# Kernel tuning notes

Measured on AMD Instinct MI355X. Metric: run time of the kernel, lower is better.

Reference implementation:

```python
import jax, jax.numpy as jnp
import numpy as np

B, DIM, D_IN, HID, N_HID_EXTRA = 65536, 128, 64, 512, 2  # num_hidden_layers=3 -> 2 extra hidden linears
LOG_SCALE_CLAMP = 2.0


def _mlp(x, Win, bin_, Whid, bhid, Wout, bout):
    # torch nn.Linear: y = x @ W.T + b
    h = jax.nn.relu(x @ Win.T + bin_)
    for i in range(Whid.shape[0]):  # fixed small layer loop
        h = jax.nn.relu(h @ Whid[i].T + bhid[i])
    return h @ Wout.T + bout


def setup_inputs() -> dict:
    key = jax.random.key(0)
    ks = jax.random.split(key, 13)
    w = lambda k, shp: (jax.random.normal(k, shp, dtype=jnp.float32) * 0.05)
    d_out = DIM - D_IN
    return {
        "z": jax.random.normal(ks[0], (B, DIM), dtype=jnp.float32),
        "s_Win": w(ks[1], (HID, D_IN)),   "s_bin": jnp.zeros((HID,), jnp.float32),
        "s_Whid": w(ks[2], (N_HID_EXTRA, HID, HID)), "s_bhid": jnp.zeros((N_HID_EXTRA, HID), jnp.float32),
        "s_Wout": w(ks[3], (d_out, HID)), "s_bout": jnp.zeros((d_out,), jnp.float32),
        "t_Win": w(ks[4], (HID, D_IN)),   "t_bin": jnp.zeros((HID,), jnp.float32),
        "t_Whid": w(ks[5], (N_HID_EXTRA, HID, HID)), "t_bhid": jnp.zeros((N_HID_EXTRA, HID), jnp.float32),
        "t_Wout": w(ks[6], (d_out, HID)), "t_bout": jnp.zeros((d_out,), jnp.float32),
    }


def reference(z, s_Win, s_bin, s_Whid, s_bhid, s_Wout, s_bout,
              t_Win, t_bin, t_Whid, t_bhid, t_Wout, t_bout):
    # mask = first D_IN dims -> gather reduces to slicing
    z1 = z[:, :D_IN]   # (B, d_in)  passthrough half
    z2 = z[:, D_IN:]   # (B, d_out) transformed half
    log_s = jnp.clip(_mlp(z1, s_Win, s_bin, s_Whid, s_bhid, s_Wout, s_bout),
                     -LOG_SCALE_CLAMP, LOG_SCALE_CLAMP)
    t = _mlp(z1, t_Win, t_bin, t_Whid, t_bhid, t_Wout, t_bout)
    z2_out = z2 * jnp.exp(log_s) + t
    z_out = jnp.concatenate([z1, z2_out], axis=1)  # scatter back per mask
    log_det = log_s.sum(axis=-1)                   # (B,)
    return (z_out, log_det)
```

## Files before the change

### kernel.cpp

```cpp
#include <hip/hip_runtime.h>
#include <stdint.h>


#define NROWS 65536
#define RPB   64
#define NBLK  (NROWS / RPB)

#define OFF_S_WIN   0
#define OFF_S_WHID  32768
#define OFF_S_WOUT  557056
#define OFF_T_WIN   589824
#define OFF_T_WHID  622592
#define OFF_T_WOUT  1146880
#define W_ELEMS     1179648

#define P_SCR  0
#define SC2    17408

typedef __attribute__((ext_vector_type(8)))  short short8;
typedef __attribute__((ext_vector_type(4)))  float f32x4;
typedef __attribute__((ext_vector_type(16))) float f32x16;

__device__ __forceinline__ uint32_t f2bf1(float f) {
  uint32_t u = __float_as_uint(f);
  return (u + 0x7fffu + ((u >> 16) & 1u)) >> 16;
}
__device__ __forceinline__ uint32_t pk2bf(float a, float b) {
  return f2bf1(a) | (f2bf1(b) << 16);
}

__global__ void cvt_weights(const float* __restrict__ sWin, const float* __restrict__ sWhid,
                            const float* __restrict__ sWout, const float* __restrict__ tWin,
                            const float* __restrict__ tWhid, const float* __restrict__ tWout,
                            uint16_t* __restrict__ wbf) {
  int g = blockIdx.x * blockDim.x + threadIdx.x;
  int e = g * 4;
  if (e >= W_ELEMS) return;
  const float* src; int off, base; bool k64;
  if      (e < OFF_S_WHID) { src = sWin;  off = e;              base = OFF_S_WIN;  k64 = true; }
  else if (e < OFF_S_WOUT) { src = sWhid; off = e - OFF_S_WHID; base = OFF_S_WHID; k64 = false; }
  else if (e < OFF_T_WIN)  { src = sWout; off = e - OFF_S_WOUT; base = OFF_S_WOUT; k64 = false; }
  else if (e < OFF_T_WHID) { src = tWin;  off = e - OFF_T_WIN;  base = OFF_T_WIN;  k64 = true; }
  else if (e < OFF_T_WOUT) { src = tWhid; off = e - OFF_T_WHID; base = OFF_T_WHID; k64 = false; }
  else                     { src = tWout; off = e - OFF_T_WOUT; base = OFF_T_WOUT; k64 = false; }
  int m, k, tsz;
  if (k64) { m = off >> 6; k = off & 63;  tsz = 2048;  }
  else     { m = off >> 9; k = off & 511; tsz = 16384; }
  int dest = base + (m >> 5) * tsz + (k >> 3) * 256 + (m & 31) * 8 + (k & 7);
  f32x4 v = *(const f32x4*)(src + off);
  uint2 r; r.x = pk2bf(v.x, v.y); r.y = pk2bf(v.z, v.w);
  *(uint2*)(wbf + dest) = r;
}

template<bool BF>
__device__ __forceinline__ short8 ldW(const uint16_t* __restrict__ wb,
                                      const float* __restrict__ wf, int pidx, int oidx) {
  if (BF) {
    return *(const short8*)(wb + pidx);
  } else {
    f32x4 x = *(const f32x4*)(wf + oidx);
    f32x4 y = *(const f32x4*)(wf + oidx + 4);
    short8 r;
    r[0] = (short)f2bf1(x.x); r[1] = (short)f2bf1(x.y);
    r[2] = (short)f2bf1(x.z); r[3] = (short)f2bf1(x.w);
    r[4] = (short)f2bf1(y.x); r[5] = (short)f2bf1(y.y);
    r[6] = (short)f2bf1(y.z); r[7] = (short)f2bf1(y.w);
    return r;
  }
}

__device__ __forceinline__ void store_h32(f32x16 acc[2][2], const float* __restrict__ bias,
                                          uint16_t* hdst, int wave, int lane) {
  const int l31 = lane & 31, lh = lane >> 5;
  __syncthreads();
  char* wp = (char*)hdst + wave * 8192 + l31 * 16 + lh * 8;
  #pragma unroll
  for (int nt = 0; nt < 2; ++nt) {
    #pragma unroll
    for (int q = 0; q < 4; ++q) {
      const int m0 = wave * 64 + nt * 32 + q * 8 + lh * 4;
      f32x4 bv = *(const f32x4*)(bias + m0);
      #pragma unroll
      for (int rt = 0; rt < 2; ++rt) {
        float v0 = acc[nt][rt][q * 4 + 0] + bv.x;
        float v1 = acc[nt][rt][q * 4 + 1] + bv.y;
        float v2 = acc[nt][rt][q * 4 + 2] + bv.z;
        float v3 = acc[nt][rt][q * 4 + 3] + bv.w;
        uint2 p;
        p.x = pk2bf(fmaxf(v0, 0.f), fmaxf(v1, 0.f));
        p.y = pk2bf(fmaxf(v2, 0.f), fmaxf(v3, 0.f));
        *(uint2*)(wp + nt * 4096 + q * 1024 + rt * 512) = p;
      }
    }
  }
  __syncthreads();
}

template<bool BF>
__device__ __forceinline__ void dense_in(
    const uint16_t* __restrict__ wb, const float* __restrict__ wf,
    const float* __restrict__ bias, const float* __restrict__ z, long rowbase,
    uint16_t* hdst, int wave, int lane) {
  const int l31 = lane & 31, lh = lane >> 5;
  f32x16 acc[2][2];
  #pragma unroll
  for (int i = 0; i < 2; ++i)
    #pragma unroll
    for (int j = 0; j < 2; ++j) acc[i][j] = (f32x16)0.f;
  #pragma unroll 1
  for (int ks = 0; ks < 4; ++ks) {
    short8 a[2];
    #pragma unroll
    for (int nt = 0; nt < 2; ++nt)
      a[nt] = ldW<BF>(wb, wf,
                      (wave * 2 + nt) * 2048 + (2 * ks + lh) * 256 + l31 * 8,
                      (wave * 64 + nt * 32 + l31) * 64 + ks * 16 + lh * 8);
    #pragma unroll
    for (int rt = 0; rt < 2; ++rt) {
      const float* zp = z + (rowbase + rt * 32 + l31) * 128 + ks * 16 + lh * 8;
      f32x4 u = *(const f32x4*)zp;
      f32x4 v = *(const f32x4*)(zp + 4);
      short8 b;
      b[0] = (short)f2bf1(u.x); b[1] = (short)f2bf1(u.y);
      b[2] = (short)f2bf1(u.z); b[3] = (short)f2bf1(u.w);
      b[4] = (short)f2bf1(v.x); b[5] = (short)f2bf1(v.y);
      b[6] = (short)f2bf1(v.z); b[7] = (short)f2bf1(v.w);
      #pragma unroll
      for (int nt = 0; nt < 2; ++nt)
        acc[nt][rt] = __builtin_amdgcn_mfma_f32_32x32x16_bf16(a[nt], b, acc[nt][rt], 0, 0, 0);
    }
  }
  store_h32(acc, bias, hdst, wave, lane);
}

template<bool BF>
__device__ __forceinline__ void dense_relu512(
    const uint16_t* __restrict__ wb, const float* __restrict__ wf,
    const float* __restrict__ bias, uint16_t* hbuf, int wave, int lane) {
  const int l31 = lane & 31, lh = lane >> 5;
  f32x16 acc[2][2];
  #pragma unroll
  for (int i = 0; i < 2; ++i)
    #pragma unroll
    for (int j = 0; j < 2; ++j) acc[i][j] = (f32x16)0.f;
  const int wbaseP = wave * 2 * 16384 + lh * 256 + l31 * 8;
  const int wbaseO = (wave * 64 + l31) * 512 + lh * 8;
  const char* bb = (const char*)hbuf + l31 * 16 + lh * 1024;

  short8 aA[2], aB[2], bA[2], bB[2];
  aA[0] = ldW<BF>(wb, wf, wbaseP, wbaseO);
  aA[1] = ldW<BF>(wb, wf, wbaseP + 16384, wbaseO + 16384);
  bA[0] = *(const short8*)(bb);
  bA[1] = *(const short8*)(bb + 512);

  #pragma unroll 1
  for (int c = 0; c < 8; ++c) {
    const char* bc = bb + c * 8192;
    const int kc = c * 4;
    #pragma unroll
    for (int j = 0; j < 4; ++j) {
      const int ks = kc + j;
      const int kp = (ks + 1 > 31) ? 31 : (ks + 1);
      aB[0] = ldW<BF>(wb, wf, wbaseP + kp * 512,         wbaseO + kp * 16);
      aB[1] = ldW<BF>(wb, wf, wbaseP + 16384 + kp * 512, wbaseO + 16384 + kp * 16);
      bB[0] = *(const short8*)(bc + (j + 1) * 2048);
      bB[1] = *(const short8*)(bc + (j + 1) * 2048 + 512);
      __builtin_amdgcn_s_setprio(1);
      acc[0][0] = __builtin_amdgcn_mfma_f32_32x32x16_bf16(aA[0], bA[0], acc[0][0], 0, 0, 0);
      acc[0][1] = __builtin_amdgcn_mfma_f32_32x32x16_bf16(aA[0], bA[1], acc[0][1], 0, 0, 0);
      acc[1][0] = __builtin_amdgcn_mfma_f32_32x32x16_bf16(aA[1], bA[0], acc[1][0], 0, 0, 0);
      acc[1][1] = __builtin_amdgcn_mfma_f32_32x32x16_bf16(aA[1], bA[1], acc[1][1], 0, 0, 0);
      __builtin_amdgcn_s_setprio(0);
      aA[0] = aB[0]; aA[1] = aB[1];
      bA[0] = bB[0]; bA[1] = bB[1];
    }
  }
  store_h32(acc, bias, hbuf, wave, lane);
}

template<bool BF>
__device__ __forceinline__ void final_partial(
    const uint16_t* __restrict__ wb, const float* __restrict__ wf,
    const uint16_t* hbuf, int nt, int rt, int kh, int lane, f32x16& acc) {
  const int l31 = lane & 31, lh = lane >> 5;
  acc = (f32x16)0.f;
  #pragma unroll 1
  for (int c = 0; c < 4; ++c) {
    #pragma unroll
    for (int j = 0; j < 4; ++j) {
      const int ks = c * 4 + j;
      const int kt = 2 * (kh * 16 + ks) + lh;
      short8 a = ldW<BF>(wb, wf, nt * 16384 + kt * 256 + l31 * 8,
                         (nt * 32 + l31) * 512 + kh * 256 + ks * 16 + lh * 8);
      short8 b = *(const short8*)((const char*)hbuf + kt * 1024 + (rt * 32 + l31) * 16);
      acc = __builtin_amdgcn_mfma_f32_32x32x16_bf16(a, b, acc, 0, 0, 0);
    }
  }
}

template<bool BF>
__global__ __launch_bounds__(512, 4) void coupling(
    const float* __restrict__ z,
    const float* __restrict__ sWin, const float* __restrict__ sbin,
    const float* __restrict__ sWhid, const float* __restrict__ sbhid,
    const float* __restrict__ sWout, const float* __restrict__ sbout,
    const float* __restrict__ tWin, const float* __restrict__ tbin,
    const float* __restrict__ tWhid, const float* __restrict__ tbhid,
    const float* __restrict__ tWout, const float* __restrict__ tbout,
    const uint16_t* __restrict__ wbf, float* __restrict__ out) {
  extern __shared__ __align__(16) uint16_t h[];
  const int tid = threadIdx.x;
  const int wave = tid >> 6, lane = tid & 63;
  const int l31 = lane & 31, lh = lane >> 5;
  const long rowbase = (long)blockIdx.x * RPB;
  const int fnt = wave & 1, frt = (wave >> 1) & 1, fkh = wave >> 2;

  dense_in<BF>(wbf + OFF_S_WIN, sWin, sbin, z, rowbase, h, wave, lane);
  dense_relu512<BF>(wbf + OFF_S_WHID, sWhid, sbhid, h, wave, lane);
  dense_relu512<BF>(wbf + OFF_S_WHID + 262144, sWhid + 262144, sbhid + 512, h, wave, lane);

  #pragma unroll
  for (int i = 0; i < 2; ++i) {
    int v = tid + i * 512;
    int row = v >> 4, kc = (v & 15) * 4;
    *(f32x4*)(out + (rowbase + row) * 128 + kc) =
        *(const f32x4*)(z + (rowbase + row) * 128 + kc);
  }

  {
    f32x16 fa;
    final_partial<BF>(wbf + OFF_S_WOUT, sWout, h, fnt, frt, fkh, lane, fa);
    __syncthreads();
    char* sc = (char*)h + P_SCR + (fnt * 2 + frt) * 4352 + lane * 68;
    if (fkh) {
      #pragma unroll
      for (int q = 0; q < 4; ++q)
        *(f32x4*)(sc + q * 16) = (f32x4){fa[q * 4], fa[q * 4 + 1], fa[q * 4 + 2], fa[q * 4 + 3]};
    }
    __syncthreads();
    if (!fkh) {
      const long row = rowbase + frt * 32 + l31;
      float sum = 0.f;
      #pragma unroll
      for (int q = 0; q < 4; ++q) {
        f32x4 p = *(const f32x4*)(sc + q * 16);
        const int m0 = fnt * 32 + q * 8 + lh * 4;
        f32x4 bv = *(const f32x4*)(sbout + m0);
        f32x4 v;
        v.x = fminf(fmaxf(fa[q * 4 + 0] + p.x + bv.x, -2.f), 2.f);
        v.y = fminf(fmaxf(fa[q * 4 + 1] + p.y + bv.y, -2.f), 2.f);
        v.z = fminf(fmaxf(fa[q * 4 + 2] + p.z + bv.z, -2.f), 2.f);
        v.w = fminf(fmaxf(fa[q * 4 + 3] + p.w + bv.w, -2.f), 2.f);
        sum += v.x + v.y + v.z + v.w;
        *(f32x4*)(out + row * 128 + 64 + m0) = v;
      }
      sum += __shfl_xor(sum, 32, 64);
      if (lane < 32)
        *(float*)((char*)h + SC2 + (fnt * 64 + frt * 32 + l31) * 4) = sum;
    }
    __syncthreads();
    if ((wave == 0 || wave == 2) && lane < 32) {
      float t0 = *(const float*)((char*)h + SC2 + (frt * 32 + l31) * 4);
      float t1 = *(const float*)((char*)h + SC2 + (64 + frt * 32 + l31) * 4);
      out[(long)NROWS * 128 + rowbase + frt * 32 + l31] = t0 + t1;
    }
  }
  __syncthreads();

  dense_in<BF>(wbf + OFF_T_WIN, tWin, tbin, z, rowbase, h, wave, lane);
  dense_relu512<BF>(wbf + OFF_T_WHID, tWhid, tbhid, h, wave, lane);
  dense_relu512<BF>(wbf + OFF_T_WHID + 262144, tWhid + 262144, tbhid + 512, h, wave, lane);

  {
    f32x16 fa;
    final_partial<BF>(wbf + OFF_T_WOUT, tWout, h, fnt, frt, fkh, lane, fa);
    __syncthreads();
    char* sc = (char*)h + P_SCR + (fnt * 2 + frt) * 4352 + lane * 68;
    if (fkh) {
      #pragma unroll
      for (int q = 0; q < 4; ++q)
        *(f32x4*)(sc + q * 16) = (f32x4){fa[q * 4], fa[q * 4 + 1], fa[q * 4 + 2], fa[q * 4 + 3]};
    }
    __syncthreads();
    if (!fkh) {
      const long row = rowbase + frt * 32 + l31;
      #pragma unroll
      for (int q = 0; q < 4; ++q) {
        f32x4 p = *(const f32x4*)(sc + q * 16);
        const int m0 = fnt * 32 + q * 8 + lh * 4;
        f32x4 bv = *(const f32x4*)(tbout + m0);
        f32x4 tv;
        tv.x = fa[q * 4 + 0] + p.x + bv.x;
        tv.y = fa[q * 4 + 1] + p.y + bv.y;
        tv.z = fa[q * 4 + 2] + p.z + bv.z;
        tv.w = fa[q * 4 + 3] + p.w + bv.w;
        const long o = row * 128 + 64 + m0;
        f32x4 ls = *(const f32x4*)(out + o);
        f32x4 z2 = *(const f32x4*)(z + o);
        f32x4 r;
        r.x = z2.x * __expf(ls.x) + tv.x;
        r.y = z2.y * __expf(ls.y) + tv.y;
        r.z = z2.z * __expf(ls.z) + tv.z;
        r.w = z2.w * __expf(ls.w) + tv.w;
        *(f32x4*)(out + o) = r;
      }
    }
  }
}

extern "C" void kernel_launch(void* const* d_in, const int* in_sizes, int n_in,
                              void* d_out, int out_size, void* d_ws, size_t ws_size,
                              hipStream_t stream) {
  const float* z     = (const float*)d_in[0];
  const float* sWin  = (const float*)d_in[1];
  const float* sbin  = (const float*)d_in[2];
  const float* sWhid = (const float*)d_in[3];
  const float* sbhid = (const float*)d_in[4];
  const float* sWout = (const float*)d_in[5];
  const float* sbout = (const float*)d_in[6];
  const float* tWin  = (const float*)d_in[7];
  const float* tbin  = (const float*)d_in[8];
  const float* tWhid = (const float*)d_in[9];
  const float* tbhid = (const float*)d_in[10];
  const float* tWout = (const float*)d_in[11];
  const float* tbout = (const float*)d_in[12];
  float* out = (float*)d_out;
  const size_t lds_bytes = 69632;

  if (ws_size >= (size_t)W_ELEMS * sizeof(uint16_t)) {
    uint16_t* wbf = (uint16_t*)d_ws;
    cvt_weights<<<W_ELEMS / 4 / 256, 256, 0, stream>>>(sWin, sWhid, sWout, tWin, tWhid, tWout, wbf);
    coupling<true><<<NBLK, 512, lds_bytes, stream>>>(z, sWin, sbin, sWhid, sbhid, sWout, sbout,
                                                     tWin, tbin, tWhid, tbhid, tWout, tbout, wbf, out);
  } else {
    coupling<false><<<NBLK, 512, lds_bytes, stream>>>(z, sWin, sbin, sWhid, sbhid, sWout, sbout,
                                                      tWin, tbin, tWhid, tbhid, tWout, tbout,
                                                      (const uint16_t*)d_in[1], out);
  }
}
```

Baseline: 192.0 us.

## Double rows per block to 128 for greater weight reuse per MFMA tile

Each block now handles 128 rows instead of 64. Every wave holds a 2x4 grid of 32x32 accumulators, so each weight fragment loaded feeds four MFMAs instead of two. The hidden-layer loop is hand-unrolled with ping-pong register buffers, and the output layer is remapped so each wave covers both column tiles, which removes the extra log-det reduction pass through LDS. In exchange, LDS use doubles to 139 KB, register pressure rises, and the launch bound drops to 2 blocks per CU.

```diff
diff --git a/kernel.cpp b/kernel.cpp
--- a/kernel.cpp
+++ b/kernel.cpp
@@ -3,7 +3,7 @@
 
 
 #define NROWS 65536
-#define RPB   64
+#define RPB   128
 #define NBLK  (NROWS / RPB)
 
 #define OFF_S_WIN   0
@@ -13,9 +13,6 @@
 #define OFF_T_WHID  622592
 #define OFF_T_WOUT  1146880
 #define W_ELEMS     1179648
-
-#define P_SCR  0
-#define SC2    17408
 
 typedef __attribute__((ext_vector_type(8)))  short short8;
 typedef __attribute__((ext_vector_type(4)))  float f32x4;
@@ -69,11 +66,13 @@
   }
 }
 
-__device__ __forceinline__ void store_h32(f32x16 acc[2][2], const float* __restrict__ bias,
+#define MFMA32(a, b, c) __builtin_amdgcn_mfma_f32_32x32x16_bf16(a, b, c, 0, 0, 0)
+
+__device__ __forceinline__ void store_h32(f32x16 acc[2][4], const float* __restrict__ bias,
                                           uint16_t* hdst, int wave, int lane) {
   const int l31 = lane & 31, lh = lane >> 5;
   __syncthreads();
-  char* wp = (char*)hdst + wave * 8192 + l31 * 16 + lh * 8;
+  char* wp = (char*)hdst + wave * 16384 + l31 * 16 + lh * 8;
   #pragma unroll
   for (int nt = 0; nt < 2; ++nt) {
     #pragma unroll
@@ -81,7 +80,7 @@
       const int m0 = wave * 64 + nt * 32 + q * 8 + lh * 4;
       f32x4 bv = *(const f32x4*)(bias + m0);
       #pragma unroll
-      for (int rt = 0; rt < 2; ++rt) {
+      for (int rt = 0; rt < 4; ++rt) {
         float v0 = acc[nt][rt][q * 4 + 0] + bv.x;
         float v1 = acc[nt][rt][q * 4 + 1] + bv.y;
         float v2 = acc[nt][rt][q * 4 + 2] + bv.z;
@@ -89,7 +88,7 @@
         uint2 p;
         p.x = pk2bf(fmaxf(v0, 0.f), fmaxf(v1, 0.f));
         p.y = pk2bf(fmaxf(v2, 0.f), fmaxf(v3, 0.f));
-        *(uint2*)(wp + nt * 4096 + q * 1024 + rt * 512) = p;
+        *(uint2*)(wp + nt * 8192 + q * 2048 + rt * 512) = p;
       }
     }
   }
@@ -102,21 +101,19 @@
     const float* __restrict__ bias, const float* __restrict__ z, long rowbase,
     uint16_t* hdst, int wave, int lane) {
   const int l31 = lane & 31, lh = lane >> 5;
-  f32x16 acc[2][2];
+  f32x16 acc[2][4];
   #pragma unroll
   for (int i = 0; i < 2; ++i)
     #pragma unroll
-    for (int j = 0; j < 2; ++j) acc[i][j] = (f32x16)0.f;
+    for (int j = 0; j < 4; ++j) acc[i][j] = (f32x16)0.f;
   #pragma unroll 1
   for (int ks = 0; ks < 4; ++ks) {
-    short8 a[2];
-    #pragma unroll
-    for (int nt = 0; nt < 2; ++nt)
-      a[nt] = ldW<BF>(wb, wf,
-                      (wave * 2 + nt) * 2048 + (2 * ks + lh) * 256 + l31 * 8,
-                      (wave * 64 + nt * 32 + l31) * 64 + ks * 16 + lh * 8);
-    #pragma unroll
-    for (int rt = 0; rt < 2; ++rt) {
+    short8 a0 = ldW<BF>(wb, wf, (wave * 2 + 0) * 2048 + (2 * ks + lh) * 256 + l31 * 8,
+                        (wave * 64 + 0 + l31) * 64 + ks * 16 + lh * 8);
+    short8 a1 = ldW<BF>(wb, wf, (wave * 2 + 1) * 2048 + (2 * ks + lh) * 256 + l31 * 8,
+                        (wave * 64 + 32 + l31) * 64 + ks * 16 + lh * 8);
+    #pragma unroll
+    for (int rt = 0; rt < 4; ++rt) {
       const float* zp = z + (rowbase + rt * 32 + l31) * 128 + ks * 16 + lh * 8;
       f32x4 u = *(const f32x4*)zp;
       f32x4 v = *(const f32x4*)(zp + 4);
@@ -125,55 +122,71 @@
       b[2] = (short)f2bf1(u.z); b[3] = (short)f2bf1(u.w);
       b[4] = (short)f2bf1(v.x); b[5] = (short)f2bf1(v.y);
       b[6] = (short)f2bf1(v.z); b[7] = (short)f2bf1(v.w);
-      #pragma unroll
-      for (int nt = 0; nt < 2; ++nt)
-        acc[nt][rt] = __builtin_amdgcn_mfma_f32_32x32x16_bf16(a[nt], b, acc[nt][rt], 0, 0, 0);
+      acc[0][rt] = MFMA32(a0, b, acc[0][rt]);
+      acc[1][rt] = MFMA32(a1, b, acc[1][rt]);
     }
   }
   store_h32(acc, bias, hdst, wave, lane);
 }
+
+#define HSTEP(AC0, AC1, BC0, BC1, BC2, BC3, AN0, AN1, BN0, BN1, BN2, BN3, AOFF, BOFF) \
+  AN0 = ldW<BF>(wb, wf, wpc + (AOFF),         woc + (AOFF) / 32);                     \
+  AN1 = ldW<BF>(wb, wf, wpc + 16384 + (AOFF), woc + 16384 + (AOFF) / 32);             \
+  BN0 = *(const short8*)(bc + (BOFF));                                                \
+  BN1 = *(const short8*)(bc + (BOFF) + 512);                                          \
+  BN2 = *(const short8*)(bc + (BOFF) + 1024);                                         \
+  BN3 = *(const short8*)(bc + (BOFF) + 1536);                                         \
+  __builtin_amdgcn_s_setprio(1);                                                      \
+  acc[0][0] = MFMA32(AC0, BC0, acc[0][0]);                                            \
+  acc[0][1] = MFMA32(AC0, BC1, acc[0][1]);                                            \
+  acc[0][2] = MFMA32(AC0, BC2, acc[0][2]);                                            \
+  acc[0][3] = MFMA32(AC0, BC3, acc[0][3]);                                            \
+  acc[1][0] = MFMA32(AC1, BC0, acc[1][0]);                                            \
+  acc[1][1] = MFMA32(AC1, BC1, acc[1][1]);                                            \
+  acc[1][2] = MFMA32(AC1, BC2, acc[1][2]);                                            \
+  acc[1][3] = MFMA32(AC1, BC3, acc[1][3]);                                            \
+  __builtin_amdgcn_s_setprio(0);
 
 template<bool BF>
 __device__ __forceinline__ void dense_relu512(
     const uint16_t* __restrict__ wb, const float* __restrict__ wf,
     const float* __restrict__ bias, uint16_t* hbuf, int wave, int lane) {
   const int l31 = lane & 31, lh = lane >> 5;
-  f32x16 acc[2][2];
+  f32x16 acc[2][4];
   #pragma unroll
   for (int i = 0; i < 2; ++i)
     #pragma unroll
-    for (int j = 0; j < 2; ++j) acc[i][j] = (f32x16)0.f;
+    for (int j = 0; j < 4; ++j) acc[i][j] = (f32x16)0.f;
   const int wbaseP = wave * 2 * 16384 + lh * 256 + l31 * 8;
   const int wbaseO = (wave * 64 + l31) * 512 + lh * 8;
-  const char* bb = (const char*)hbuf + l31 * 16 + lh * 1024;
-
-  short8 aA[2], aB[2], bA[2], bB[2];
-  aA[0] = ldW<BF>(wb, wf, wbaseP, wbaseO);
-  aA[1] = ldW<BF>(wb, wf, wbaseP + 16384, wbaseO + 16384);
-  bA[0] = *(const short8*)(bb);
-  bA[1] = *(const short8*)(bb + 512);
+  const char* bb = (const char*)hbuf + lh * 2048 + l31 * 16;
+
+  short8 aC0, aC1, aN0, aN1, bC0, bC1, bC2, bC3, bN0, bN1, bN2, bN3;
+  aC0 = ldW<BF>(wb, wf, wbaseP, wbaseO);
+  aC1 = ldW<BF>(wb, wf, wbaseP + 16384, wbaseO + 16384);
+  bC0 = *(const short8*)(bb);
+  bC1 = *(const short8*)(bb + 512);
+  bC2 = *(const short8*)(bb + 1024);
+  bC3 = *(const short8*)(bb + 1536);
 
   #pragma unroll 1
-  for (int c = 0; c < 8; ++c) {
-    const char* bc = bb + c * 8192;
-    const int kc = c * 4;
-    #pragma unroll
-    for (int j = 0; j < 4; ++j) {
-      const int ks = kc + j;
-      const int kp = (ks + 1 > 31) ? 31 : (ks + 1);
-      aB[0] = ldW<BF>(wb, wf, wbaseP + kp * 512,         wbaseO + kp * 16);
-      aB[1] = ldW<BF>(wb, wf, wbaseP + 16384 + kp * 512, wbaseO + 16384 + kp * 16);
-      bB[0] = *(const short8*)(bc + (j + 1) * 2048);
-      bB[1] = *(const short8*)(bc + (j + 1) * 2048 + 512);
-      __builtin_amdgcn_s_setprio(1);
-      acc[0][0] = __builtin_amdgcn_mfma_f32_32x32x16_bf16(aA[0], bA[0], acc[0][0], 0, 0, 0);
-      acc[0][1] = __builtin_amdgcn_mfma_f32_32x32x16_bf16(aA[0], bA[1], acc[0][1], 0, 0, 0);
-      acc[1][0] = __builtin_amdgcn_mfma_f32_32x32x16_bf16(aA[1], bA[0], acc[1][0], 0, 0, 0);
-      acc[1][1] = __builtin_amdgcn_mfma_f32_32x32x16_bf16(aA[1], bA[1], acc[1][1], 0, 0, 0);
-      __builtin_amdgcn_s_setprio(0);
-      aA[0] = aB[0]; aA[1] = aB[1];
-      bA[0] = bB[0]; bA[1] = bB[1];
-    }
+  for (int c = 0; c < 7; ++c) {
+    const int   wpc = wbaseP + c * 2048;
+    const int   woc = wbaseO + c * 64;
+    const char* bc  = bb + c * 16384;
+    HSTEP(aC0, aC1, bC0, bC1, bC2, bC3, aN0, aN1, bN0, bN1, bN2, bN3, 1 * 512, 1 * 4096)
+    HSTEP(aN0, aN1, bN0, bN1, bN2, bN3, aC0, aC1, bC0, bC1, bC2, bC3, 2 * 512, 2 * 4096)
+    HSTEP(aC0, aC1, bC0, bC1, bC2, bC3, aN0, aN1, bN0, bN1, bN2, bN3, 3 * 512, 3 * 4096)
+    HSTEP(aN0, aN1, bN0, bN1, bN2, bN3, aC0, aC1, bC0, bC1, bC2, bC3, 4 * 512, 4 * 4096)
+  }
+  {
+    const int   wpc = wbaseP + 7 * 2048;
+    const int   woc = wbaseO + 7 * 64;
+    const char* bc  = bb + 7 * 16384;
+    HSTEP(aC0, aC1, bC0, bC1, bC2, bC3, aN0, aN1, bN0, bN1, bN2, bN3, 1 * 512, 1 * 4096)
+    HSTEP(aN0, aN1, bN0, bN1, bN2, bN3, aC0, aC1, bC0, bC1, bC2, bC3, 2 * 512, 2 * 4096)
+    HSTEP(aC0, aC1, bC0, bC1, bC2, bC3, aN0, aN1, bN0, bN1, bN2, bN3, 3 * 512, 3 * 4096)
+    HSTEP(aN0, aN1, bN0, bN1, bN2, bN3, aC0, aC1, bC0, bC1, bC2, bC3, 3 * 512, 4 * 4096)
   }
   store_h32(acc, bias, hbuf, wave, lane);
 }
@@ -181,25 +194,28 @@
 template<bool BF>
 __device__ __forceinline__ void final_partial(
     const uint16_t* __restrict__ wb, const float* __restrict__ wf,
-    const uint16_t* hbuf, int nt, int rt, int kh, int lane, f32x16& acc) {
-  const int l31 = lane & 31, lh = lane >> 5;
-  acc = (f32x16)0.f;
+    const uint16_t* hbuf, int frt, int fkh, int lane, f32x16 fa[2]) {
+  const int l31 = lane & 31, lh = lane >> 5;
+  fa[0] = (f32x16)0.f; fa[1] = (f32x16)0.f;
+  const int aP = fkh * 8192 + lh * 256 + l31 * 8;
+  const int aO = l31 * 512 + fkh * 256 + lh * 8;
+  const char* fb = (const char*)hbuf + fkh * 65536 + lh * 2048 + (frt * 32 + l31) * 16;
   #pragma unroll 1
   for (int c = 0; c < 4; ++c) {
     #pragma unroll
     for (int j = 0; j < 4; ++j) {
       const int ks = c * 4 + j;
-      const int kt = 2 * (kh * 16 + ks) + lh;
-      short8 a = ldW<BF>(wb, wf, nt * 16384 + kt * 256 + l31 * 8,
-                         (nt * 32 + l31) * 512 + kh * 256 + ks * 16 + lh * 8);
-      short8 b = *(const short8*)((const char*)hbuf + kt * 1024 + (rt * 32 + l31) * 16);
-      acc = __builtin_amdgcn_mfma_f32_32x32x16_bf16(a, b, acc, 0, 0, 0);
-    }
-  }
-}
-
-template<bool BF>
-__global__ __launch_bounds__(512, 4) void coupling(
+      short8 b  = *(const short8*)(fb + ks * 4096);
+      short8 a0 = ldW<BF>(wb, wf, aP + ks * 512,         aO + ks * 16);
+      short8 a1 = ldW<BF>(wb, wf, aP + 16384 + ks * 512, aO + 16384 + ks * 16);
+      fa[0] = MFMA32(a0, b, fa[0]);
+      fa[1] = MFMA32(a1, b, fa[1]);
+    }
+  }
+}
+
+template<bool BF>
+__global__ __launch_bounds__(512, 2) void coupling(
     const float* __restrict__ z,
     const float* __restrict__ sWin, const float* __restrict__ sbin,
     const float* __restrict__ sWhid, const float* __restrict__ sbhid,
@@ -213,14 +229,14 @@
   const int wave = tid >> 6, lane = tid & 63;
   const int l31 = lane & 31, lh = lane >> 5;
   const long rowbase = (long)blockIdx.x * RPB;
-  const int fnt = wave & 1, frt = (wave >> 1) & 1, fkh = wave >> 2;
+  const int frt = wave & 3, fkh = wave >> 2;
 
   dense_in<BF>(wbf + OFF_S_WIN, sWin, sbin, z, rowbase, h, wave, lane);
   dense_relu512<BF>(wbf + OFF_S_WHID, sWhid, sbhid, h, wave, lane);
   dense_relu512<BF>(wbf + OFF_S_WHID + 262144, sWhid + 262144, sbhid + 512, h, wave, lane);
 
   #pragma unroll
-  for (int i = 0; i < 2; ++i) {
+  for (int i = 0; i < 4; ++i) {
     int v = tid + i * 512;
     int row = v >> 4, kc = (v & 15) * 4;
     *(f32x4*)(out + (rowbase + row) * 128 + kc) =
@@ -228,41 +244,40 @@
   }
 
   {
-    f32x16 fa;
-    final_partial<BF>(wbf + OFF_S_WOUT, sWout, h, fnt, frt, fkh, lane, fa);
+    f32x16 fa[2];
+    final_partial<BF>(wbf + OFF_S_WOUT, sWout, h, frt, fkh, lane, fa);
     __syncthreads();
-    char* sc = (char*)h + P_SCR + (fnt * 2 + frt) * 4352 + lane * 68;
+    char* sc = (char*)h + frt * 8192 + lane * 128;
     if (fkh) {
       #pragma unroll
-      for (int q = 0; q < 4; ++q)
-        *(f32x4*)(sc + q * 16) = (f32x4){fa[q * 4], fa[q * 4 + 1], fa[q * 4 + 2], fa[q * 4 + 3]};
+      for (int nt = 0; nt < 2; ++nt)
+        #pragma unroll
+        for (int q = 0; q < 4; ++q)
+          *(f32x4*)(sc + nt * 64 + q * 16) =
+              (f32x4){fa[nt][q * 4], fa[nt][q * 4 + 1], fa[nt][q * 4 + 2], fa[nt][q * 4 + 3]};
     }
     __syncthreads();
     if (!fkh) {
       const long row = rowbase + frt * 32 + l31;
       float sum = 0.f;
       #pragma unroll
-      for (int q = 0; q < 4; ++q) {
-        f32x4 p = *(const f32x4*)(sc + q * 16);
-        const int m0 = fnt * 32 + q * 8 + lh * 4;
-        f32x4 bv = *(const f32x4*)(sbout + m0);
-        f32x4 v;
-        v.x = fminf(fmaxf(fa[q * 4 + 0] + p.x + bv.x, -2.f), 2.f);
-        v.y = fminf(fmaxf(fa[q * 4 + 1] + p.y + bv.y, -2.f), 2.f);
-        v.z = fminf(fmaxf(fa[q * 4 + 2] + p.z + bv.z, -2.f), 2.f);
-        v.w = fminf(fmaxf(fa[q * 4 + 3] + p.w + bv.w, -2.f), 2.f);
-        sum += v.x + v.y + v.z + v.w;
-        *(f32x4*)(out + row * 128 + 64 + m0) = v;
+      for (int nt = 0; nt < 2; ++nt) {
+        #pragma unroll
+        for (int q = 0; q < 4; ++q) {
+          f32x4 p = *(const f32x4*)(sc + nt * 64 + q * 16);
+          const int m0 = nt * 32 + q * 8 + lh * 4;
+          f32x4 bv = *(const f32x4*)(sbout + m0);
+          f32x4 v;
+          v.x = fminf(fmaxf(fa[nt][q * 4 + 0] + p.x + bv.x, -2.f), 2.f);
+          v.y = fminf(fmaxf(fa[nt][q * 4 + 1] + p.y + bv.y, -2.f), 2.f);
+          v.z = fminf(fmaxf(fa[nt][q * 4 + 2] + p.z + bv.z, -2.f), 2.f);
+          v.w = fminf(fmaxf(fa[nt][q * 4 + 3] + p.w + bv.w, -2.f), 2.f);
+          sum += v.x + v.y + v.z + v.w;
+          *(f32x4*)(out + row * 128 + 64 + m0) = v;
+        }
       }
       sum += __shfl_xor(sum, 32, 64);
-      if (lane < 32)
-        *(float*)((char*)h + SC2 + (fnt * 64 + frt * 32 + l31) * 4) = sum;
-    }
-    __syncthreads();
-    if ((wave == 0 || wave == 2) && lane < 32) {
-      float t0 = *(const float*)((char*)h + SC2 + (frt * 32 + l31) * 4);
-      float t1 = *(const float*)((char*)h + SC2 + (64 + frt * 32 + l31) * 4);
-      out[(long)NROWS * 128 + rowbase + frt * 32 + l31] = t0 + t1;
+      if (lane < 32) out[(long)NROWS * 128 + row] = sum;
     }
   }
   __syncthreads();
@@ -272,37 +287,43 @@
   dense_relu512<BF>(wbf + OFF_T_WHID + 262144, tWhid + 262144, tbhid + 512, h, wave, lane);
 
   {
-    f32x16 fa;
-    final_partial<BF>(wbf + OFF_T_WOUT, tWout, h, fnt, frt, fkh, lane, fa);
+    f32x16 fa[2];
+    final_partial<BF>(wbf + OFF_T_WOUT, tWout, h, frt, fkh, lane, fa);
     __syncthreads();
-    char* sc = (char*)h + P_SCR + (fnt * 2 + frt) * 4352 + lane * 68;
+    char* sc = (char*)h + frt * 8192 + lane * 128;
     if (fkh) {
       #pragma unroll
-      for (int q = 0; q < 4; ++q)
-        *(f32x4*)(sc + q * 16) = (f32x4){fa[q * 4], fa[q * 4 + 1], fa[q * 4 + 2], fa[q * 4 + 3]};
+      for (int nt = 0; nt < 2; ++nt)
+        #pragma unroll
+        for (int q = 0; q < 4; ++q)
+          *(f32x4*)(sc + nt * 64 + q * 16) =
+              (f32x4){fa[nt][q * 4], fa[nt][q * 4 + 1], fa[nt][q * 4 + 2], fa[nt][q * 4 + 3]};
     }
     __syncthreads();
     if (!fkh) {
       const long row = rowbase + frt * 32 + l31;
       #pragma unroll
-      for (int q = 0; q < 4; ++q) {
-        f32x4 p = *(const f32x4*)(sc + q * 16);
-        const int m0 = fnt * 32 + q * 8 + lh * 4;
-        f32x4 bv = *(const f32x4*)(tbout + m0);
-        f32x4 tv;
-        tv.x = fa[q * 4 + 0] + p.x + bv.x;
-        tv.y = fa[q * 4 + 1] + p.y + bv.y;
-        tv.z = fa[q * 4 + 2] + p.z + bv.z;
-        tv.w = fa[q * 4 + 3] + p.w + bv.w;
-        const long o = row * 128 + 64 + m0;
-        f32x4 ls = *(const f32x4*)(out + o);
-        f32x4 z2 = *(const f32x4*)(z + o);
-        f32x4 r;
-        r.x = z2.x * __expf(ls.x) + tv.x;
-        r.y = z2.y * __expf(ls.y) + tv.y;
-        r.z = z2.z * __expf(ls.z) + tv.z;
-        r.w = z2.w * __expf(ls.w) + tv.w;
-        *(f32x4*)(out + o) = r;
+      for (int nt = 0; nt < 2; ++nt) {
+        #pragma unroll
+        for (int q = 0; q < 4; ++q) {
+          f32x4 p = *(const f32x4*)(sc + nt * 64 + q * 16);
+          const int m0 = nt * 32 + q * 8 + lh * 4;
+          f32x4 bv = *(const f32x4*)(tbout + m0);
+          f32x4 tv;
+          tv.x = fa[nt][q * 4 + 0] + p.x + bv.x;
+          tv.y = fa[nt][q * 4 + 1] + p.y + bv.y;
+          tv.z = fa[nt][q * 4 + 2] + p.z + bv.z;
+          tv.w = fa[nt][q * 4 + 3] + p.w + bv.w;
+          const long o = row * 128 + 64 + m0;
+          f32x4 ls = *(const f32x4*)(out + o);
+          f32x4 z2 = *(const f32x4*)(z + o);
+          f32x4 r;
+          r.x = z2.x * __expf(ls.x) + tv.x;
+          r.y = z2.y * __expf(ls.y) + tv.y;
+          r.z = z2.z * __expf(ls.z) + tv.z;
+          r.w = z2.w * __expf(ls.w) + tv.w;
+          *(f32x4*)(out + o) = r;
+        }
       }
     }
   }
@@ -325,7 +346,7 @@
   const float* tWout = (const float*)d_in[11];
   const float* tbout = (const float*)d_in[12];
   float* out = (float*)d_out;
-  const size_t lds_bytes = 69632;
+  const size_t lds_bytes = 139264;
 
   if (ws_size >= (size_t)W_ELEMS * sizeof(uint16_t)) {
     uint16_t* wbf = (uint16_t*)d_ws;
```

Result: no change. 194.5 us (+1.3%).
